# Kernel tuning notes

Measured on AMD Instinct MI355X. Metric: run time of the kernel, lower is better.

The kernel has to match this reference:

```python
import jax, jax.numpy as jnp
import numpy as np

N = 50000
E = 800000
IN_CH = 256
OUT_CH = 64   # per-head channels (PyG out_channels)
HEADS = 4
NEG_SLOPE = 0.2


def setup_inputs() -> dict:
    key = jax.random.key(0)
    k = jax.random.split(key, 8)
    x = jax.random.normal(k[0], (N, IN_CH), dtype=jnp.float32)
    edge_index = jax.random.randint(k[1], (2, E), 0, N, dtype=jnp.int64)
    # GATConv parameters
    W = jax.random.normal(k[2], (IN_CH, HEADS * OUT_CH), dtype=jnp.float32) * (1.0 / np.sqrt(IN_CH))
    att_src = jax.random.normal(k[3], (HEADS, OUT_CH), dtype=jnp.float32) * 0.1
    att_dst = jax.random.normal(k[4], (HEADS, OUT_CH), dtype=jnp.float32) * 0.1
    bias = jnp.zeros((OUT_CH,), dtype=jnp.float32)
    # residual linear (bias=False)
    W_res = jax.random.normal(k[5], (IN_CH, OUT_CH), dtype=jnp.float32) * (1.0 / np.sqrt(IN_CH))
    return {"x": x, "edge_index": edge_index, "W": W, "att_src": att_src,
            "att_dst": att_dst, "bias": bias, "W_res": W_res}


def _gat_forward(x, edge_index, W, att_src, att_dst, bias, W_res):
    # residual branch
    x_res = x @ W_res                                   # [N, OUT_CH]

    # node transform: [N, H, C]
    xw = (x @ W).reshape(N, HEADS, OUT_CH)
    # per-node attention logits, [N, H]
    a_src = jnp.einsum('nhc,hc->nh', xw, att_src)
    a_dst = jnp.einsum('nhc,hc->nh', xw, att_dst)

    # add self-loops (PyG GATConv default add_self_loops=True)
    loops = jnp.arange(N, dtype=edge_index.dtype)
    src = jnp.concatenate([edge_index[0], loops])       # [E+N]
    dst = jnp.concatenate([edge_index[1], loops])       # [E+N]

    # per-edge logits + leaky relu, [E+N, H]
    alpha = jax.nn.leaky_relu(a_src[src] + a_dst[dst], NEG_SLOPE)

    # segment softmax over destination nodes
    m = jax.ops.segment_max(alpha, dst, num_segments=N)    # [N, H]
    e = jnp.exp(alpha - m[dst])
    denom = jax.ops.segment_sum(e, dst, num_segments=N)    # [N, H]
    a = e / denom[dst]                                     # [E+N, H]
    # (dropout p=0.1 on attention coeffs is identity in eval mode)

    # weighted scatter-aggregate: [N, H, C]
    msgs = xw[src] * a[:, :, None]
    out = jax.ops.segment_sum(msgs, dst, num_segments=N)

    # concat=False -> mean over heads, then bias
    x_conv = out.mean(axis=1) + bias                     # [N, OUT_CH]
    return jax.nn.relu(x_conv + x_res)


def reference(x, edge_index, W, att_src, att_dst, bias, W_res):
    return _gat_forward(x, edge_index, W, att_src, att_dst, bias, W_res)
```

## Files before the change

kernel.cpp:

```cpp
#include <hip/hip_runtime.h>
#include <math.h>

#define N_NODES 50000
#define N_EDGES 800000
#define IN_CH   256
#define OUT_CH  64
#define HEADS   4
#define NEG_SLOPE 0.2f
#define NCOLS   320
#define NTILES  20
#define NKK     8
#define PACK_BLOCKS 40
#define GEMM_BLOCKS 782
#define NBINS   782
#define P1_BLOCKS 256
#define EPB     3125
#define AGG_BLOCKS 12500
#define STASH_CAP 1280

typedef __attribute__((ext_vector_type(8))) short short8;
typedef __attribute__((ext_vector_type(4))) float f32x4;

__device__ __forceinline__ float lrelu(float v) {
    return v > 0.f ? v : NEG_SLOPE * v;
}
__device__ __forceinline__ unsigned bf16_rne(float f) {
    unsigned u = __float_as_uint(f);
    return (u + 0x7FFFu + ((u >> 16) & 1u)) >> 16;
}
__device__ __forceinline__ unsigned pack2(float lo, float hi) {
    return bf16_rne(lo) | (bf16_rne(hi) << 16);
}
__device__ __forceinline__ float bflo(unsigned u) { return __uint_as_float(u << 16); }
__device__ __forceinline__ float bfhi(unsigned u) { return __uint_as_float(u & 0xFFFF0000u); }
__device__ __forceinline__ short8 as_short8(uint4 u) {
    union { uint4 u4; short8 s8; } cv; cv.u4 = u; return cv.s8;
}

__global__ __launch_bounds__(256) void prep(
    const int* __restrict__ ei, int* __restrict__ M,
    const float* __restrict__ W, const float* __restrict__ Wres,
    uint4* __restrict__ Bp)
{
    __shared__ int lh[NBINS];
    const int t = threadIdx.x;

    if (blockIdx.x < P1_BLOCKS) {
        const int blk = blockIdx.x;
        for (int b = t; b < NBINS; b += 256) lh[b] = 0;
        __syncthreads();
        const int e0 = blk * EPB;
        #pragma unroll
        for (int r = 0; r < 13; ++r) {
            const int idx = (r << 8) + t;
            if (idx < EPB)
                atomicAdd(&lh[ei[N_EDGES + e0 + idx] >> 6], 1);
        }
        __syncthreads();
        for (int b = t; b < NBINS; b += 256)
            M[(size_t)b * P1_BLOCKS + blk] = lh[b];
        return;
    }

    const int idx  = (blockIdx.x - P1_BLOCKS) * 256 + t;
    const int kk   = idx / (NTILES * 64);
    const int rem  = idx - kk * (NTILES * 64);
    const int tt   = rem >> 6;
    const int lane = rem & 63;
    const int colL = lane & 15, quad = lane >> 4;
    const int col  = tt * 16 + colL;
    const int k0   = kk * 32 + quad * 8;
    float v[8];
    #pragma unroll
    for (int j = 0; j < 8; ++j) {
        const int k = k0 + j;
        v[j] = (col < IN_CH) ? W[(size_t)k * IN_CH + col]
                             : Wres[(size_t)k * OUT_CH + (col - IN_CH)];
    }
    uint4 u;
    u.x = pack2(v[0], v[1]); u.y = pack2(v[2], v[3]);
    u.z = pack2(v[4], v[5]); u.w = pack2(v[6], v[7]);
    Bp[(kk * NTILES + tt) * 64 + lane] = u;
}

__global__ __launch_bounds__(256) void binscan_M(
    int* __restrict__ M, int* __restrict__ binCnt)
{
    __shared__ int ws[4];
    const int t = threadIdx.x, lane = t & 63, w = t >> 6;
    const int b = blockIdx.x;
    const int v = M[(size_t)b * P1_BLOCKS + t];
    int sc = v;
    #pragma unroll
    for (int off = 1; off < 64; off <<= 1) {
        const int n = __shfl_up(sc, off);
        if (lane >= off) sc += n;
    }
    if (lane == 63) ws[w] = sc;
    __syncthreads();
    int prefix = 0;
    for (int j = 0; j < w; ++j) prefix += ws[j];
    M[(size_t)b * P1_BLOCKS + t] = prefix + sc - v;
    if (t == 255) binCnt[b] = prefix + sc;
}

__device__ __forceinline__ void gemm_body(
    const int n0, const float* __restrict__ x, const uint4* __restrict__ Bp,
    uint2* __restrict__ xw2, float* __restrict__ xres,
    const float* __restrict__ attS, const float* __restrict__ attD,
    float* __restrict__ asrc, float* __restrict__ adst,
    uint4* Alds, float (*logS)[HEADS], float (*logD)[HEADS])
{
    const int tid = threadIdx.x;

    logS[tid >> 2][tid & 3] = 0.f;
    logD[tid >> 2][tid & 3] = 0.f;

    #pragma unroll
    for (int i = 0; i < 8; ++i) {
        const int e    = i * 256 + tid;
        const int g    = e >> 9;
        const int kk   = (e >> 6) & 7;
        const int lane = e & 63;
        const int cL   = lane & 15, qd = lane >> 4;
        const int row  = n0 + g * 16 + cL;
        const int k0   = kk * 32 + qd * 8;
        uint4 u = make_uint4(0u, 0u, 0u, 0u);
        if (row < N_NODES) {
            const float4 a = *reinterpret_cast<const float4*>(x + (size_t)row * IN_CH + k0);
            const float4 b = *reinterpret_cast<const float4*>(x + (size_t)row * IN_CH + k0 + 4);
            u.x = pack2(a.x, a.y); u.y = pack2(a.z, a.w);
            u.z = pack2(b.x, b.y); u.w = pack2(b.z, b.w);
        }
        Alds[(g * NKK + kk) * 64 + lane] = u;
    }
    __syncthreads();

    const int lane = tid & 63;
    const int wv   = tid >> 6;
    const int colL = lane & 15, quad = lane >> 4;

    f32x4 acc[4][5];
    #pragma unroll
    for (int rg = 0; rg < 4; ++rg)
        #pragma unroll
        for (int j = 0; j < 5; ++j) acc[rg][j] = (f32x4){0.f, 0.f, 0.f, 0.f};

    for (int kk = 0; kk < NKK; ++kk) {
        uint4 bu[5];
        #pragma unroll
        for (int j = 0; j < 5; ++j)
            bu[j] = Bp[(kk * NTILES + j * 4 + wv) * 64 + lane];
        #pragma unroll
        for (int rg = 0; rg < 4; ++rg) {
            const short8 a = as_short8(Alds[(rg * NKK + kk) * 64 + lane]);
            #pragma unroll
            for (int j = 0; j < 5; ++j)
                acc[rg][j] = __builtin_amdgcn_mfma_f32_16x16x32_bf16(
                    a, as_short8(bu[j]), acc[rg][j], 0, 0, 0);
        }
    }

    #pragma unroll
    for (int rg = 0; rg < 4; ++rg) {
        #pragma unroll
        for (int r = 0; r < 4; ++r) {
            const int row = n0 + rg * 16 + quad * 4 + r;
            if (row < N_NODES) {
                xw2[(size_t)row * 64 + wv * 16 + colL] = make_uint2(
                    pack2(acc[rg][0][r], acc[rg][1][r]),
                    pack2(acc[rg][2][r], acc[rg][3][r]));
                xres[(size_t)row * OUT_CH + wv * 16 + colL] = acc[rg][4][r];
            }
        }
    }

    float aSr[HEADS], aDr[HEADS];
    #pragma unroll
    for (int h = 0; h < HEADS; ++h) {
        aSr[h] = attS[h * 64 + wv * 16 + colL];
        aDr[h] = attD[h * 64 + wv * 16 + colL];
    }
    #pragma unroll
    for (int rg = 0; rg < 4; ++rg) {
        #pragma unroll
        for (int h = 0; h < HEADS; ++h) {
            #pragma unroll
            for (int r = 0; r < 4; ++r) {
                float vS = acc[rg][h][r] * aSr[h];
                float vD = acc[rg][h][r] * aDr[h];
                #pragma unroll
                for (int m = 1; m < 16; m <<= 1) {
                    vS += __shfl_xor(vS, m);
                    vD += __shfl_xor(vD, m);
                }
                if (colL == 0) {
                    atomicAdd(&logS[rg * 16 + quad * 4 + r][h], vS);
                    atomicAdd(&logD[rg * 16 + quad * 4 + r][h], vD);
                }
            }
        }
    }
    __syncthreads();
    {
        const int rl = tid >> 2, h = tid & 3;
        const int row = n0 + rl;
        if (row < N_NODES) {
            asrc[(size_t)row * HEADS + h] = logS[rl][h];
            adst[(size_t)row * HEADS + h] = logD[rl][h];
        }
    }
}

__global__ __launch_bounds__(256) void gemm_part(
    const float* __restrict__ x, const uint4* __restrict__ Bp,
    uint2* __restrict__ xw2, float* __restrict__ xres,
    const float* __restrict__ attS, const float* __restrict__ attD,
    float* __restrict__ asrc, float* __restrict__ adst,
    const int* __restrict__ ei, const int* __restrict__ M,
    const int* __restrict__ binCnt, int* __restrict__ binStart,
    unsigned* __restrict__ mid)
{
    __shared__ uint4 Alds[4 * NKK * 64];
    __shared__ float logS[64][HEADS];
    __shared__ float logD[64][HEADS];
    const int t = threadIdx.x, lane = t & 63, wv = t >> 6;

    if (blockIdx.x < P1_BLOCKS) {
        int* bc    = (int*)Alds;
        int* bs    = bc + NBINS;
        int* baseL = bs + NBINS;
        int* lh    = baseL + NBINS;
        int* ws    = lh + NBINS;
        const int blk = blockIdx.x;

        for (int b = t; b < NBINS; b += 256) {
            bc[b] = binCnt[b];
            baseL[b] = M[(size_t)b * P1_BLOCKS + blk];
            lh[b] = 0;
        }
        __syncthreads();

        int carry = 0;
        for (int c = 0; c < 4; ++c) {
            const int i = (c << 8) + t;
            const int v = (i < NBINS) ? bc[i] : 0;
            int sc = v;
            #pragma unroll
            for (int o = 1; o < 64; o <<= 1) {
                const int n = __shfl_up(sc, o);
                if (lane >= o) sc += n;
            }
            if (lane == 63) ws[wv] = sc;
            __syncthreads();
            int prefix = 0;
            for (int j = 0; j < wv; ++j) prefix += ws[j];
            if (i < NBINS) bs[i] = carry + prefix + sc - v;
            carry += ws[0] + ws[1] + ws[2] + ws[3];
            __syncthreads();
        }
        for (int b = t; b < NBINS; b += 256) baseL[b] += bs[b];
        if (blk == 0)
            for (int b = t; b < NBINS; b += 256) binStart[b] = bs[b];
        __syncthreads();

        const int e0 = blk * EPB;
        #pragma unroll
        for (int r = 0; r < 13; ++r) {
            const int idx = (r << 8) + t;
            if (idx < EPB) {
                const int e = e0 + idx;
                const int d = ei[N_EDGES + e];
                const int b = d >> 6;
                const int pos = atomicAdd(&lh[b], 1);
                mid[baseL[b] + pos] = ((unsigned)(d & 63) << 17) | (unsigned)ei[e];
            }
        }
        return;
    }
    gemm_body((blockIdx.x - P1_BLOCKS) * 64,
              x, Bp, xw2, xres, attS, attD, asrc, adst, Alds, logS, logD);
}

__global__ __launch_bounds__(256) void scatter_fine2(
    const unsigned* __restrict__ mid, const int* __restrict__ binStart,
    const int* __restrict__ binCnt,
    int* __restrict__ cnt, int* __restrict__ lscan, int* __restrict__ esrc)
{
    __shared__ int c64[64];
    __shared__ int o64[64];
    __shared__ unsigned stash[STASH_CAP];
    const int t = threadIdx.x;
    const int b = blockIdx.x;

    const int base = binStart[b];
    const int n = binCnt[b];
    if (t < 64) c64[t] = 0;
    __syncthreads();

    for (int i = t; i < n; i += 256) {
        const unsigned m = mid[base + i];
        if (i < STASH_CAP) stash[i] = m;
        atomicAdd(&c64[m >> 17], 1);
    }
    __syncthreads();

    if (t < 64) {
        const int v = c64[t];
        int sc = v;
        #pragma unroll
        for (int o = 1; o < 64; o <<= 1) {
            const int nn = __shfl_up(sc, o);
            if (t >= o) sc += nn;
        }
        const int ex = sc - v;
        o64[t] = ex;
        const int d = (b << 6) + t;
        if (d < N_NODES) {
            cnt[d] = v;
            lscan[d] = base + ex;
        }
        c64[t] = 0;
    }
    __syncthreads();

    for (int i = t; i < n; i += 256) {
        const unsigned m = (i < STASH_CAP) ? stash[i] : mid[base + i];
        const int dlo = (int)(m >> 17);
        const int pos = atomicAdd(&c64[dlo], 1);
        esrc[base + o64[dlo] + pos] = (int)(m & 0x1FFFFu);
    }
}

__global__ __launch_bounds__(256) void aggregate(
    const int* __restrict__ esrc, const int* __restrict__ lscan,
    const int* __restrict__ cnt,
    const float* __restrict__ asrc, const float* __restrict__ adst,
    const uint2* __restrict__ xw2, const float* __restrict__ xres,
    const float* __restrict__ bias, float* __restrict__ out)
{
    __shared__ float4 wbuf[4][64];
    __shared__ int    sbuf[4][64];
    const int t = threadIdx.x;
    const int lane = t & 63;
    const int wv   = t >> 6;

    const int d = blockIdx.x * 4 + wv;
    const int row = lscan[d];
    const int deg = cnt[d];
    const float4 ad = *reinterpret_cast<const float4*>(adst + (size_t)d * 4);
    const char* xwB = (const char*)xw2;
    const int laneB = lane << 3;

    float dn0 = 0.f, dn1 = 0.f, dn2 = 0.f, dn3 = 0.f;
    float ac0 = 0.f, ac1 = 0.f, ac2 = 0.f, ac3 = 0.f;

    for (int base = 0; base < deg; base += 64) {
        const int m = min(64, deg - base);
        if (lane < m) {
            const int s = esrc[row + base + lane];
            const float4 as = *reinterpret_cast<const float4*>(asrc + (size_t)s * 4);
            const float e0 = __expf(lrelu(as.x + ad.x));
            const float e1 = __expf(lrelu(as.y + ad.y));
            const float e2 = __expf(lrelu(as.z + ad.z));
            const float e3 = __expf(lrelu(as.w + ad.w));
            dn0 += e0; dn1 += e1; dn2 += e2; dn3 += e3;
            wbuf[wv][lane] = make_float4(e0, e1, e2, e3);
            sbuf[wv][lane] = s << 9;
        }
        int j = 0;
        for (; j + 4 <= m; j += 4) {
            uint2 v0 = *(const uint2*)(xwB + sbuf[wv][j]     + laneB);
            uint2 v1 = *(const uint2*)(xwB + sbuf[wv][j + 1] + laneB);
            uint2 v2 = *(const uint2*)(xwB + sbuf[wv][j + 2] + laneB);
            uint2 v3 = *(const uint2*)(xwB + sbuf[wv][j + 3] + laneB);
            {
                const float4 w = wbuf[wv][j];
                ac0 = fmaf(w.x, bflo(v0.x), ac0); ac1 = fmaf(w.y, bfhi(v0.x), ac1);
                ac2 = fmaf(w.z, bflo(v0.y), ac2); ac3 = fmaf(w.w, bfhi(v0.y), ac3);
            }
            {
                const float4 w = wbuf[wv][j + 1];
                ac0 = fmaf(w.x, bflo(v1.x), ac0); ac1 = fmaf(w.y, bfhi(v1.x), ac1);
                ac2 = fmaf(w.z, bflo(v1.y), ac2); ac3 = fmaf(w.w, bfhi(v1.y), ac3);
            }
            {
                const float4 w = wbuf[wv][j + 2];
                ac0 = fmaf(w.x, bflo(v2.x), ac0); ac1 = fmaf(w.y, bfhi(v2.x), ac1);
                ac2 = fmaf(w.z, bflo(v2.y), ac2); ac3 = fmaf(w.w, bfhi(v2.y), ac3);
            }
            {
                const float4 w = wbuf[wv][j + 3];
                ac0 = fmaf(w.x, bflo(v3.x), ac0); ac1 = fmaf(w.y, bfhi(v3.x), ac1);
                ac2 = fmaf(w.z, bflo(v3.y), ac2); ac3 = fmaf(w.w, bfhi(v3.y), ac3);
            }
        }
        for (; j < m; ++j) {
            const float4 w = wbuf[wv][j];
            const uint2 v = *(const uint2*)(xwB + sbuf[wv][j] + laneB);
            ac0 = fmaf(w.x, bflo(v.x), ac0);
            ac1 = fmaf(w.y, bfhi(v.x), ac1);
            ac2 = fmaf(w.z, bflo(v.y), ac2);
            ac3 = fmaf(w.w, bfhi(v.y), ac3);
        }
    }

    #pragma unroll
    for (int off = 32; off >= 1; off >>= 1) {
        dn0 += __shfl_xor(dn0, off);
        dn1 += __shfl_xor(dn1, off);
        dn2 += __shfl_xor(dn2, off);
        dn3 += __shfl_xor(dn3, off);
    }
    const float4 asd = *reinterpret_cast<const float4*>(asrc + (size_t)d * 4);
    const float s0 = __expf(lrelu(asd.x + ad.x));
    const float s1 = __expf(lrelu(asd.y + ad.y));
    const float s2 = __expf(lrelu(asd.z + ad.z));
    const float s3 = __expf(lrelu(asd.w + ad.w));
    const uint2 u = xw2[(size_t)d * 64 + lane];
    ac0 = fmaf(s0, bflo(u.x), ac0); ac1 = fmaf(s1, bfhi(u.x), ac1);
    ac2 = fmaf(s2, bflo(u.y), ac2); ac3 = fmaf(s3, bfhi(u.y), ac3);
    const float i0 = 0.25f / (dn0 + s0);
    const float i1 = 0.25f / (dn1 + s1);
    const float i2 = 0.25f / (dn2 + s2);
    const float i3 = 0.25f / (dn3 + s3);
    const float v = ac0 * i0 + ac1 * i1 + ac2 * i2 + ac3 * i3
                  + bias[lane] + xres[(size_t)d * OUT_CH + lane];
    out[(size_t)d * OUT_CH + lane] = fmaxf(v, 0.f);
}

extern "C" void kernel_launch(void* const* d_in, const int* in_sizes, int n_in,
                              void* d_out, int out_size, void* d_ws, size_t ws_size,
                              hipStream_t stream) {
    const float* x    = (const float*)d_in[0];
    const int*   ei   = (const int*)d_in[1];
    const float* W    = (const float*)d_in[2];
    const float* attS = (const float*)d_in[3];
    const float* attD = (const float*)d_in[4];
    const float* bias = (const float*)d_in[5];
    const float* Wres = (const float*)d_in[6];
    float* out = (float*)d_out;

    char* p = (char*)d_ws;
    uint4*    Bp      = (uint4*)p;    p += (size_t)NKK * NTILES * 64 * 16;
    uint2*    xw2     = (uint2*)p;    p += (size_t)N_NODES * 64 * 8;
    float*    xres    = (float*)p;    p += (size_t)N_NODES * OUT_CH * 4;
    float*    asrc    = (float*)p;    p += (size_t)N_NODES * HEADS * 4;
    float*    adst    = (float*)p;    p += (size_t)N_NODES * HEADS * 4;
    int*      M       = (int*)p;      p += (size_t)NBINS * P1_BLOCKS * 4;
    int*      binCnt  = (int*)p;      p += 1024 * 4;
    int*      binStart= (int*)p;      p += 1024 * 4;
    int*      cnt     = (int*)p;      p += (size_t)N_NODES * 4;
    int*      lscan   = (int*)p;      p += (size_t)N_NODES * 4;
    unsigned* mid     = (unsigned*)p; p += (size_t)N_EDGES * 4;
    int*      esrc    = (int*)p;      p += (size_t)N_EDGES * 4;

    prep<<<P1_BLOCKS + PACK_BLOCKS, 256, 0, stream>>>(ei, M, W, Wres, Bp);
    binscan_M<<<NBINS, 256, 0, stream>>>(M, binCnt);
    gemm_part<<<P1_BLOCKS + GEMM_BLOCKS, 256, 0, stream>>>(
        x, Bp, xw2, xres, attS, attD, asrc, adst, ei, M, binCnt, binStart, mid);
    scatter_fine2<<<NBINS, 256, 0, stream>>>(
        mid, binStart, binCnt, cnt, lscan, esrc);
    aggregate<<<AGG_BLOCKS, 256, 0, stream>>>(
        esrc, lscan, cnt, asrc, adst, xw2, xres, bias, out);
}
```

Before: 224.1 us.

## Fuse bin scan into partition kernel and merge fine sort with aggregation

```diff
diff --git a/kernel.cpp b/kernel.cpp
--- a/kernel.cpp
+++ b/kernel.cpp
@@ -15,8 +15,7 @@
 #define NBINS   782
 #define P1_BLOCKS 256
 #define EPB     3125
-#define AGG_BLOCKS 12500
-#define STASH_CAP 1280
+#define SORT_CAP 1600
 
 typedef __attribute__((ext_vector_type(8))) short short8;
 typedef __attribute__((ext_vector_type(4))) float f32x4;
@@ -81,27 +80,6 @@
     u.x = pack2(v[0], v[1]); u.y = pack2(v[2], v[3]);
     u.z = pack2(v[4], v[5]); u.w = pack2(v[6], v[7]);
     Bp[(kk * NTILES + tt) * 64 + lane] = u;
-}
-
-__global__ __launch_bounds__(256) void binscan_M(
-    int* __restrict__ M, int* __restrict__ binCnt)
-{
-    __shared__ int ws[4];
-    const int t = threadIdx.x, lane = t & 63, w = t >> 6;
-    const int b = blockIdx.x;
-    const int v = M[(size_t)b * P1_BLOCKS + t];
-    int sc = v;
-    #pragma unroll
-    for (int off = 1; off < 64; off <<= 1) {
-        const int n = __shfl_up(sc, off);
-        if (lane >= off) sc += n;
-    }
-    if (lane == 63) ws[w] = sc;
-    __syncthreads();
-    int prefix = 0;
-    for (int j = 0; j < w; ++j) prefix += ws[j];
-    M[(size_t)b * P1_BLOCKS + t] = prefix + sc - v;
-    if (t == 255) binCnt[b] = prefix + sc;
 }
 
 __device__ __forceinline__ void gemm_body(
@@ -212,13 +190,13 @@
     }
 }
 
-__global__ __launch_bounds__(256) void gemm_part(
+__global__ __launch_bounds__(256) void gemm_part2(
     const float* __restrict__ x, const uint4* __restrict__ Bp,
     uint2* __restrict__ xw2, float* __restrict__ xres,
     const float* __restrict__ attS, const float* __restrict__ attD,
     float* __restrict__ asrc, float* __restrict__ adst,
     const int* __restrict__ ei, const int* __restrict__ M,
-    const int* __restrict__ binCnt, int* __restrict__ binStart,
+    int* __restrict__ binCnt, int* __restrict__ binStart,
     unsigned* __restrict__ mid)
 {
     __shared__ uint4 Alds[4 * NKK * 64];
@@ -234,11 +212,24 @@
         int* ws    = lh + NBINS;
         const int blk = blockIdx.x;
 
-        for (int b = t; b < NBINS; b += 256) {
-            bc[b] = binCnt[b];
-            baseL[b] = M[(size_t)b * P1_BLOCKS + blk];
-            lh[b] = 0;
-        }
+        for (int b = wv; b < NBINS; b += 4) {
+            const int* rowp = M + (size_t)b * P1_BLOCKS;
+            int tot = 0, pre = 0;
+            #pragma unroll
+            for (int c4 = 0; c4 < 4; ++c4) {
+                const int c = (c4 << 6) + lane;
+                const int v = rowp[c];
+                tot += v;
+                if (c < blk) pre += v;
+            }
+            #pragma unroll
+            for (int o = 32; o >= 1; o >>= 1) {
+                tot += __shfl_xor(tot, o);
+                pre += __shfl_xor(pre, o);
+            }
+            if (lane == 0) { bc[b] = tot; baseL[b] = pre; }
+        }
+        for (int b = t; b < NBINS; b += 256) lh[b] = 0;
         __syncthreads();
 
         int carry = 0;
@@ -260,8 +251,12 @@
             __syncthreads();
         }
         for (int b = t; b < NBINS; b += 256) baseL[b] += bs[b];
-        if (blk == 0)
-            for (int b = t; b < NBINS; b += 256) binStart[b] = bs[b];
+        if (blk == 0) {
+            for (int b = t; b < NBINS; b += 256) {
+                binStart[b] = bs[b];
+                binCnt[b]   = bc[b];
+            }
+        }
         __syncthreads();
 
         const int e0 = blk * EPB;
@@ -282,151 +277,139 @@
               x, Bp, xw2, xres, attS, attD, asrc, adst, Alds, logS, logD);
 }
 
-__global__ __launch_bounds__(256) void scatter_fine2(
+__global__ __launch_bounds__(512) void agg2(
     const unsigned* __restrict__ mid, const int* __restrict__ binStart,
     const int* __restrict__ binCnt,
-    int* __restrict__ cnt, int* __restrict__ lscan, int* __restrict__ esrc)
-{
-    __shared__ int c64[64];
-    __shared__ int o64[64];
-    __shared__ unsigned stash[STASH_CAP];
-    const int t = threadIdx.x;
-    const int b = blockIdx.x;
-
-    const int base = binStart[b];
-    const int n = binCnt[b];
-    if (t < 64) c64[t] = 0;
-    __syncthreads();
-
-    for (int i = t; i < n; i += 256) {
-        const unsigned m = mid[base + i];
-        if (i < STASH_CAP) stash[i] = m;
-        atomicAdd(&c64[m >> 17], 1);
-    }
-    __syncthreads();
-
-    if (t < 64) {
-        const int v = c64[t];
-        int sc = v;
-        #pragma unroll
-        for (int o = 1; o < 64; o <<= 1) {
-            const int nn = __shfl_up(sc, o);
-            if (t >= o) sc += nn;
-        }
-        const int ex = sc - v;
-        o64[t] = ex;
-        const int d = (b << 6) + t;
-        if (d < N_NODES) {
-            cnt[d] = v;
-            lscan[d] = base + ex;
-        }
-        c64[t] = 0;
-    }
-    __syncthreads();
-
-    for (int i = t; i < n; i += 256) {
-        const unsigned m = (i < STASH_CAP) ? stash[i] : mid[base + i];
-        const int dlo = (int)(m >> 17);
-        const int pos = atomicAdd(&c64[dlo], 1);
-        esrc[base + o64[dlo] + pos] = (int)(m & 0x1FFFFu);
-    }
-}
-
-__global__ __launch_bounds__(256) void aggregate(
-    const int* __restrict__ esrc, const int* __restrict__ lscan,
-    const int* __restrict__ cnt,
     const float* __restrict__ asrc, const float* __restrict__ adst,
     const uint2* __restrict__ xw2, const float* __restrict__ xres,
     const float* __restrict__ bias, float* __restrict__ out)
 {
-    __shared__ float4 wbuf[4][64];
-    __shared__ int    sbuf[4][64];
-    const int t = threadIdx.x;
-    const int lane = t & 63;
-    const int wv   = t >> 6;
-
-    const int d = blockIdx.x * 4 + wv;
-    const int row = lscan[d];
-    const int deg = cnt[d];
-    const float4 ad = *reinterpret_cast<const float4*>(adst + (size_t)d * 4);
+    __shared__ int c64[64];
+    __shared__ int o64[64];
+    __shared__ int srt[SORT_CAP];
+    __shared__ float4 wbuf[8][64];
+    __shared__ int    sbuf[8][64];
+    const int t = threadIdx.x, lane = t & 63, wv = t >> 6;
+    const int b = blockIdx.x;
+    const int base = binStart[b];
+    const int n = binCnt[b];
+
+    if (t < 64) c64[t] = 0;
+    __syncthreads();
+
+    for (int i = t; i < n; i += 512)
+        atomicAdd(&c64[(int)(mid[base + i] >> 17)], 1);
+    __syncthreads();
+
+    if (t < 64) {
+        const int v = c64[t];
+        int sc = v;
+        #pragma unroll
+        for (int o = 1; o < 64; o <<= 1) {
+            const int nn = __shfl_up(sc, o);
+            if (t >= o) sc += nn;
+        }
+        o64[t] = sc - v;
+        c64[t] = 0;
+    }
+    __syncthreads();
+
+    for (int i = t; i < n; i += 512) {
+        const unsigned m = mid[base + i];
+        const int dlo = (int)(m >> 17);
+        const int pos = atomicAdd(&c64[dlo], 1);
+        srt[o64[dlo] + pos] = (int)(m & 0x1FFFFu);
+    }
+    __syncthreads();
+
     const char* xwB = (const char*)xw2;
     const int laneB = lane << 3;
 
-    float dn0 = 0.f, dn1 = 0.f, dn2 = 0.f, dn3 = 0.f;
-    float ac0 = 0.f, ac1 = 0.f, ac2 = 0.f, ac3 = 0.f;
-
-    for (int base = 0; base < deg; base += 64) {
-        const int m = min(64, deg - base);
-        if (lane < m) {
-            const int s = esrc[row + base + lane];
-            const float4 as = *reinterpret_cast<const float4*>(asrc + (size_t)s * 4);
-            const float e0 = __expf(lrelu(as.x + ad.x));
-            const float e1 = __expf(lrelu(as.y + ad.y));
-            const float e2 = __expf(lrelu(as.z + ad.z));
-            const float e3 = __expf(lrelu(as.w + ad.w));
-            dn0 += e0; dn1 += e1; dn2 += e2; dn3 += e3;
-            wbuf[wv][lane] = make_float4(e0, e1, e2, e3);
-            sbuf[wv][lane] = s << 9;
-        }
-        int j = 0;
-        for (; j + 4 <= m; j += 4) {
-            uint2 v0 = *(const uint2*)(xwB + sbuf[wv][j]     + laneB);
-            uint2 v1 = *(const uint2*)(xwB + sbuf[wv][j + 1] + laneB);
-            uint2 v2 = *(const uint2*)(xwB + sbuf[wv][j + 2] + laneB);
-            uint2 v3 = *(const uint2*)(xwB + sbuf[wv][j + 3] + laneB);
-            {
+    #pragma unroll 1
+    for (int k = 0; k < 8; ++k) {
+        const int dlo = wv * 8 + k;
+        const int d = (b << 6) + dlo;
+        if (d >= N_NODES) continue;
+        const int off = o64[dlo];
+        const int deg = c64[dlo];
+        const float4 ad = *reinterpret_cast<const float4*>(adst + (size_t)d * 4);
+
+        float dn0 = 0.f, dn1 = 0.f, dn2 = 0.f, dn3 = 0.f;
+        float ac0 = 0.f, ac1 = 0.f, ac2 = 0.f, ac3 = 0.f;
+
+        for (int bs0 = 0; bs0 < deg; bs0 += 64) {
+            const int m = min(64, deg - bs0);
+            if (lane < m) {
+                const int s = srt[off + bs0 + lane];
+                const float4 as = *reinterpret_cast<const float4*>(asrc + (size_t)s * 4);
+                const float e0 = __expf(lrelu(as.x + ad.x));
+                const float e1 = __expf(lrelu(as.y + ad.y));
+                const float e2 = __expf(lrelu(as.z + ad.z));
+                const float e3 = __expf(lrelu(as.w + ad.w));
+                dn0 += e0; dn1 += e1; dn2 += e2; dn3 += e3;
+                wbuf[wv][lane] = make_float4(e0, e1, e2, e3);
+                sbuf[wv][lane] = s << 9;
+            }
+            int j = 0;
+            for (; j + 4 <= m; j += 4) {
+                uint2 v0 = *(const uint2*)(xwB + sbuf[wv][j]     + laneB);
+                uint2 v1 = *(const uint2*)(xwB + sbuf[wv][j + 1] + laneB);
+                uint2 v2 = *(const uint2*)(xwB + sbuf[wv][j + 2] + laneB);
+                uint2 v3 = *(const uint2*)(xwB + sbuf[wv][j + 3] + laneB);
+                {
+                    const float4 w = wbuf[wv][j];
+                    ac0 = fmaf(w.x, bflo(v0.x), ac0); ac1 = fmaf(w.y, bfhi(v0.x), ac1);
+                    ac2 = fmaf(w.z, bflo(v0.y), ac2); ac3 = fmaf(w.w, bfhi(v0.y), ac3);
+                }
+                {
+                    const float4 w = wbuf[wv][j + 1];
+                    ac0 = fmaf(w.x, bflo(v1.x), ac0); ac1 = fmaf(w.y, bfhi(v1.x), ac1);
+                    ac2 = fmaf(w.z, bflo(v1.y), ac2); ac3 = fmaf(w.w, bfhi(v1.y), ac3);
+                }
+                {
+                    const float4 w = wbuf[wv][j + 2];
+                    ac0 = fmaf(w.x, bflo(v2.x), ac0); ac1 = fmaf(w.y, bfhi(v2.x), ac1);
+                    ac2 = fmaf(w.z, bflo(v2.y), ac2); ac3 = fmaf(w.w, bfhi(v2.y), ac3);
+                }
+                {
+                    const float4 w = wbuf[wv][j + 3];
+                    ac0 = fmaf(w.x, bflo(v3.x), ac0); ac1 = fmaf(w.y, bfhi(v3.x), ac1);
+                    ac2 = fmaf(w.z, bflo(v3.y), ac2); ac3 = fmaf(w.w, bfhi(v3.y), ac3);
+                }
+            }
+            for (; j < m; ++j) {
                 const float4 w = wbuf[wv][j];
-                ac0 = fmaf(w.x, bflo(v0.x), ac0); ac1 = fmaf(w.y, bfhi(v0.x), ac1);
-                ac2 = fmaf(w.z, bflo(v0.y), ac2); ac3 = fmaf(w.w, bfhi(v0.y), ac3);
-            }
-            {
-                const float4 w = wbuf[wv][j + 1];
-                ac0 = fmaf(w.x, bflo(v1.x), ac0); ac1 = fmaf(w.y, bfhi(v1.x), ac1);
-                ac2 = fmaf(w.z, bflo(v1.y), ac2); ac3 = fmaf(w.w, bfhi(v1.y), ac3);
-            }
-            {
-                const float4 w = wbuf[wv][j + 2];
-                ac0 = fmaf(w.x, bflo(v2.x), ac0); ac1 = fmaf(w.y, bfhi(v2.x), ac1);
-                ac2 = fmaf(w.z, bflo(v2.y), ac2); ac3 = fmaf(w.w, bfhi(v2.y), ac3);
-            }
-            {
-                const float4 w = wbuf[wv][j + 3];
-                ac0 = fmaf(w.x, bflo(v3.x), ac0); ac1 = fmaf(w.y, bfhi(v3.x), ac1);
-                ac2 = fmaf(w.z, bflo(v3.y), ac2); ac3 = fmaf(w.w, bfhi(v3.y), ac3);
-            }
-        }
-        for (; j < m; ++j) {
-            const float4 w = wbuf[wv][j];
-            const uint2 v = *(const uint2*)(xwB + sbuf[wv][j] + laneB);
-            ac0 = fmaf(w.x, bflo(v.x), ac0);
-            ac1 = fmaf(w.y, bfhi(v.x), ac1);
-            ac2 = fmaf(w.z, bflo(v.y), ac2);
-            ac3 = fmaf(w.w, bfhi(v.y), ac3);
-        }
-    }
-
-    #pragma unroll
-    for (int off = 32; off >= 1; off >>= 1) {
-        dn0 += __shfl_xor(dn0, off);
-        dn1 += __shfl_xor(dn1, off);
-        dn2 += __shfl_xor(dn2, off);
-        dn3 += __shfl_xor(dn3, off);
-    }
-    const float4 asd = *reinterpret_cast<const float4*>(asrc + (size_t)d * 4);
-    const float s0 = __expf(lrelu(asd.x + ad.x));
-    const float s1 = __expf(lrelu(asd.y + ad.y));
-    const float s2 = __expf(lrelu(asd.z + ad.z));
-    const float s3 = __expf(lrelu(asd.w + ad.w));
-    const uint2 u = xw2[(size_t)d * 64 + lane];
-    ac0 = fmaf(s0, bflo(u.x), ac0); ac1 = fmaf(s1, bfhi(u.x), ac1);
-    ac2 = fmaf(s2, bflo(u.y), ac2); ac3 = fmaf(s3, bfhi(u.y), ac3);
-    const float i0 = 0.25f / (dn0 + s0);
-    const float i1 = 0.25f / (dn1 + s1);
-    const float i2 = 0.25f / (dn2 + s2);
-    const float i3 = 0.25f / (dn3 + s3);
-    const float v = ac0 * i0 + ac1 * i1 + ac2 * i2 + ac3 * i3
-                  + bias[lane] + xres[(size_t)d * OUT_CH + lane];
-    out[(size_t)d * OUT_CH + lane] = fmaxf(v, 0.f);
+                const uint2 v = *(const uint2*)(xwB + sbuf[wv][j] + laneB);
+                ac0 = fmaf(w.x, bflo(v.x), ac0);
+                ac1 = fmaf(w.y, bfhi(v.x), ac1);
+                ac2 = fmaf(w.z, bflo(v.y), ac2);
+                ac3 = fmaf(w.w, bfhi(v.y), ac3);
+            }
+        }
+
+        #pragma unroll
+        for (int off2 = 32; off2 >= 1; off2 >>= 1) {
+            dn0 += __shfl_xor(dn0, off2);
+            dn1 += __shfl_xor(dn1, off2);
+            dn2 += __shfl_xor(dn2, off2);
+            dn3 += __shfl_xor(dn3, off2);
+        }
+        const float4 asd = *reinterpret_cast<const float4*>(asrc + (size_t)d * 4);
+        const float s0 = __expf(lrelu(asd.x + ad.x));
+        const float s1 = __expf(lrelu(asd.y + ad.y));
+        const float s2 = __expf(lrelu(asd.z + ad.z));
+        const float s3 = __expf(lrelu(asd.w + ad.w));
+        const uint2 u = xw2[(size_t)d * 64 + lane];
+        ac0 = fmaf(s0, bflo(u.x), ac0); ac1 = fmaf(s1, bfhi(u.x), ac1);
+        ac2 = fmaf(s2, bflo(u.y), ac2); ac3 = fmaf(s3, bfhi(u.y), ac3);
+        const float i0 = 0.25f / (dn0 + s0);
+        const float i1 = 0.25f / (dn1 + s1);
+        const float i2 = 0.25f / (dn2 + s2);
+        const float i3 = 0.25f / (dn3 + s3);
+        const float v = ac0 * i0 + ac1 * i1 + ac2 * i2 + ac3 * i3
+                      + bias[lane] + xres[(size_t)d * OUT_CH + lane];
+        out[(size_t)d * OUT_CH + lane] = fmaxf(v, 0.f);
+    }
 }
 
 extern "C" void kernel_launch(void* const* d_in, const int* in_sizes, int n_in,
@@ -450,17 +433,11 @@
     int*      M       = (int*)p;      p += (size_t)NBINS * P1_BLOCKS * 4;
     int*      binCnt  = (int*)p;      p += 1024 * 4;
     int*      binStart= (int*)p;      p += 1024 * 4;
-    int*      cnt     = (int*)p;      p += (size_t)N_NODES * 4;
-    int*      lscan   = (int*)p;      p += (size_t)N_NODES * 4;
     unsigned* mid     = (unsigned*)p; p += (size_t)N_EDGES * 4;
-    int*      esrc    = (int*)p;      p += (size_t)N_EDGES * 4;
 
     prep<<<P1_BLOCKS + PACK_BLOCKS, 256, 0, stream>>>(ei, M, W, Wres, Bp);
-    binscan_M<<<NBINS, 256, 0, stream>>>(M, binCnt);
-    gemm_part<<<P1_BLOCKS + GEMM_BLOCKS, 256, 0, stream>>>(
+    gemm_part2<<<P1_BLOCKS + GEMM_BLOCKS, 256, 0, stream>>>(
         x, Bp, xw2, xres, attS, attD, asrc, adst, ei, M, binCnt, binStart, mid);
-    scatter_fine2<<<NBINS, 256, 0, stream>>>(
-        mid, binStart, binCnt, cnt, lscan, esrc);
-    aggregate<<<AGG_BLOCKS, 256, 0, stream>>>(
-        esrc, lscan, cnt, asrc, adst, xw2, xres, bias, out);
-}
+    agg2<<<NBINS, 512, 0, stream>>>(
+        mid, binStart, binCnt, asrc, adst, xw2, xres, bias, out);
+}
```

Measured after the change: 301.1 us. 34.4% more time.
